# Performance work log

Measured on AMD Instinct MI355X. Metric: run time of the kernel, lower is better.

## Reference

```python
import jax, jax.numpy as jnp
import numpy as np

HIDDEN = 128
HEADS = 8
HEAD_DIM = HIDDEN // HEADS
N = 2048
SCALE = HEAD_DIM ** -0.5


def setup_inputs() -> dict:
    key = jax.random.key(0)
    ks = jax.random.split(key, 12)
    # xavier_uniform bound for square (HIDDEN, HIDDEN) weights
    bound = float(np.sqrt(6.0 / (HIDDEN + HIDDEN)))
    def w(k):
        return jax.random.uniform(k, (HIDDEN, HIDDEN), jnp.float32, -bound, bound)
    return {
        "x": jax.random.normal(ks[0], (N, HIDDEN), jnp.float32),
        "attention_bias": jax.random.normal(ks[1], (N, N, HEADS), jnp.float32),
        "key_padding_mask": jnp.zeros((N,), jnp.bool_),
        "Wq": w(ks[2]), "bq": jnp.zeros((HIDDEN,), jnp.float32),
        "Wk": w(ks[3]), "bk": jnp.zeros((HIDDEN,), jnp.float32),
        "Wv": w(ks[4]), "bv": jnp.zeros((HIDDEN,), jnp.float32),
        "Wo": w(ks[5]), "bo": jnp.zeros((HIDDEN,), jnp.float32),
    }


def reference(x, attention_bias, key_padding_mask, Wq, bq, Wk, bk, Wv, bv, Wo, bo):
    n = x.shape[0]
    # torch Linear: y = x @ W.T + b
    q = (x @ Wq.T + bq).reshape(n, HEADS, HEAD_DIM).transpose(1, 0, 2)  # (H, N, D)
    k = (x @ Wk.T + bk).reshape(n, HEADS, HEAD_DIM).transpose(1, 0, 2)
    v = (x @ Wv.T + bv).reshape(n, HEADS, HEAD_DIM).transpose(1, 0, 2)
    scores = jnp.einsum('hnd,hmd->hnm', q, k) * SCALE        # (H, N, N)
    scores = scores + attention_bias.transpose(2, 0, 1)       # additive graph bias
    mask = key_padding_mask[None, None, :]                    # (1, 1, N) over keys
    scores = jnp.where(mask, -jnp.inf, scores)
    attn = jax.nn.softmax(scores, axis=-1)
    out = jnp.einsum('hnm,hmd->hnd', attn, v)                 # (H, N, D)
    out = out.transpose(1, 0, 2).reshape(n, HIDDEN)
    return out @ Wo.T + bo
```

## Files before the change

### kernel.cpp

```cpp
#include <hip/hip_runtime.h>
#include <hip/hip_bf16.h>

#define NSEQ 2048
#define HID 128
#define HEADS 8
#define HD 16
#define SCALE 0.25f
#define TQ 16
#define SPLIT 16
#define KEYS_PER (NSEQ / SPLIT)
#define KT16 (KEYS_PER / 16)

typedef unsigned short ushort_t;
typedef __attribute__((ext_vector_type(4))) short short4v;
typedef __attribute__((ext_vector_type(4))) float floatx4;

__device__ __forceinline__ unsigned pack_bf16x2(float a, float b) {
    __hip_bfloat16 ba = __float2bfloat16(a);
    __hip_bfloat16 bb = __float2bfloat16(b);
    return (unsigned)*(ushort_t*)&ba | ((unsigned)*(ushort_t*)&bb << 16);
}

__global__ void transpose_kernel(const float* __restrict__ Wq, const float* __restrict__ Wk,
                                 const float* __restrict__ Wv, const float* __restrict__ Wo,
                                 float* __restrict__ wt)
{
    int idx = blockIdx.x * 256 + threadIdx.x;
    int w = idx >> 14, rem = idx & 16383;
    int row = rem >> 7, col = rem & 127;
    const float* W = (w == 0) ? Wq : (w == 1) ? Wk : (w == 2) ? Wv : Wo;
    wt[w * 16384 + col * HID + row] = W[rem];
}

__global__ __launch_bounds__(128) void qkv_kernel(
    const float* __restrict__ x, const float* __restrict__ WqT,
    const float* __restrict__ WkT, const float* __restrict__ WvT,
    const float* __restrict__ bq, const float* __restrict__ bk,
    const float* __restrict__ bv,
    __hip_bfloat16* __restrict__ Qh, __hip_bfloat16* __restrict__ Ql,
    __hip_bfloat16* __restrict__ Kb, __hip_bfloat16* __restrict__ Vt)
{
    __shared__ float xs[8 * HID];
    const int j = threadIdx.x;
    const int mat = blockIdx.x >> 8;
    const int rb = blockIdx.x & 255;
    const int r0 = rb * 8;
    const float* WT = (mat == 0) ? WqT : (mat == 1) ? WkT : WvT;
    const float* bb = (mat == 0) ? bq : (mat == 1) ? bk : bv;
    const float4* xg = (const float4*)(x + (size_t)r0 * HID);
    float4* xl = (float4*)xs;
    for (int i = j; i < 8 * HID / 4; i += 128) xl[i] = xg[i];
    __syncthreads();
    float acc[8];
#pragma unroll
    for (int r = 0; r < 8; ++r) acc[r] = 0.f;
#pragma unroll 4
    for (int i = 0; i < HID; ++i) {
        float w = WT[i * HID + j];
#pragma unroll
        for (int r = 0; r < 8; ++r) acc[r] = fmaf(xs[r * HID + i], w, acc[r]);
    }
    float bv_ = bb[j];
#pragma unroll
    for (int r = 0; r < 8; ++r) acc[r] += bv_;
    if (mat == 0) {
#pragma unroll
        for (int r = 0; r < 8; ++r) {
            float qsv = acc[r] * SCALE;
            __hip_bfloat16 hb = __float2bfloat16(qsv);
            float hf = __bfloat162float(hb);
            __hip_bfloat16 lb = __float2bfloat16(qsv - hf);
            Qh[(size_t)(r0 + r) * HID + j] = hb;
            Ql[(size_t)(r0 + r) * HID + j] = lb;
        }
    } else if (mat == 1) {
#pragma unroll
        for (int r = 0; r < 8; ++r) Kb[(size_t)(r0 + r) * HID + j] = __float2bfloat16(acc[r]);
    } else {
        unsigned u[4];
#pragma unroll
        for (int p = 0; p < 4; ++p) u[p] = pack_bf16x2(acc[2 * p], acc[2 * p + 1]);
        *(uint4*)((ushort_t*)Vt + (size_t)j * NSEQ + r0) = make_uint4(u[0], u[1], u[2], u[3]);
    }
}

__global__ __launch_bounds__(256, 4) void attn_kernel(
    const __hip_bfloat16* __restrict__ Qh, const __hip_bfloat16* __restrict__ Ql,
    const __hip_bfloat16* __restrict__ Kb, const __hip_bfloat16* __restrict__ Vt,
    const float* __restrict__ bias, const unsigned char* __restrict__ mask,
    float* __restrict__ Op, float* __restrict__ Lp)
{
    const int t = threadIdx.x;
    const int lane = t & 63;
    const int wid = t >> 6;
    const int qi = lane & 15;
    const int g = lane >> 4;
    const int qb = blockIdx.x & 127;
    const int sp = blockIdx.x >> 7;
    const int n0 = qb * TQ;
    const int m0 = sp * KEYS_PER;
    const int h0 = wid * 2;

    short4v qhf[2], qlf[2];
#pragma unroll
    for (int hh = 0; hh < 2; ++hh) {
        const size_t qoff = (size_t)(n0 + qi) * HID + (h0 + hh) * HD + 4 * g;
        qhf[hh] = *(const short4v*)((const ushort_t*)Qh + qoff);
        qlf[hh] = *(const short4v*)((const ushort_t*)Ql + qoff);
    }

    floatx4 o[2];
    o[0] = (floatx4){0.f, 0.f, 0.f, 0.f};
    o[1] = (floatx4){0.f, 0.f, 0.f, 0.f};
    float lrun[2] = {0.f, 0.f};

    const float* bias_base = bias + (size_t)(n0 + qi) * NSEQ * HEADS;

#pragma unroll 2
    for (int kt = 0; kt < KT16; ++kt) {
        const int m1 = m0 + kt * 16;
        const uchar4 mk = *(const uchar4*)(mask + m1 + 4 * g);
#pragma unroll
        for (int hh = 0; hh < 2; ++hh) {
            const int h = h0 + hh;
            short4v ka = *(const short4v*)((const ushort_t*)Kb +
                         (size_t)(m1 + qi) * HID + h * HD + 4 * g);
            const float* bp = bias_base + (size_t)(m1 + 4 * g) * HEADS + h;
            floatx4 s;
            s.x = bp[0]; s.y = bp[8]; s.z = bp[16]; s.w = bp[24];
            s = __builtin_amdgcn_mfma_f32_16x16x16bf16_1k(ka, qhf[hh], s, 0, 0, 0);
            s = __builtin_amdgcn_mfma_f32_16x16x16bf16_1k(ka, qlf[hh], s, 0, 0, 0);
            float e0 = mk.x ? 0.f : __expf(s.x);
            float e1 = mk.y ? 0.f : __expf(s.y);
            float e2 = mk.z ? 0.f : __expf(s.z);
            float e3 = mk.w ? 0.f : __expf(s.w);
            lrun[hh] += (e0 + e1) + (e2 + e3);
            __hip_bfloat16 p0 = __float2bfloat16(e0);
            __hip_bfloat16 p1 = __float2bfloat16(e1);
            __hip_bfloat16 p2 = __float2bfloat16(e2);
            __hip_bfloat16 p3 = __float2bfloat16(e3);
            short4v pa = {(short)*(ushort_t*)&p0, (short)*(ushort_t*)&p1,
                          (short)*(ushort_t*)&p2, (short)*(ushort_t*)&p3};
            short4v vb = *(const short4v*)((const ushort_t*)Vt +
                         (size_t)(h * HD + qi) * NSEQ + m1 + 4 * g);
            o[hh] = __builtin_amdgcn_mfma_f32_16x16x16bf16_1k(pa, vb, o[hh], 0, 0, 0);
        }
    }

#pragma unroll
    for (int hh = 0; hh < 2; ++hh) {
        lrun[hh] += __shfl_xor(lrun[hh], 16);
        lrun[hh] += __shfl_xor(lrun[hh], 32);
        const int h = h0 + hh;
#pragma unroll
        for (int r = 0; r < 4; ++r)
            Op[((size_t)sp * NSEQ + n0 + 4 * g + r) * HID + h * HD + qi] = o[hh][r];
        if (g == 0)
            Lp[((size_t)sp * NSEQ + n0 + qi) * HEADS + h] = lrun[hh];
    }
}

__global__ __launch_bounds__(128) void proj_kernel(
    const float* __restrict__ Op, const float* __restrict__ Lp,
    const float* __restrict__ WoT, const float* __restrict__ bo,
    float* __restrict__ out)
{
    __shared__ float xs[4 * HID];
    const int j = threadIdx.x;
    const int r0 = blockIdx.x * 4;
    const int hh = j >> 4;
#pragma unroll
    for (int r = 0; r < 4; ++r) {
        const size_t n = r0 + r;
        float s = 0.f, l = 0.f;
#pragma unroll
        for (int sp = 0; sp < SPLIT; ++sp) {
            s += Op[((size_t)sp * NSEQ + n) * HID + j];
            l += Lp[((size_t)sp * NSEQ + n) * HEADS + hh];
        }
        xs[r * HID + j] = s / l;
    }
    __syncthreads();
    float acc[4];
#pragma unroll
    for (int r = 0; r < 4; ++r) acc[r] = 0.f;
#pragma unroll 4
    for (int i = 0; i < HID; ++i) {
        float w = WoT[i * HID + j];
#pragma unroll
        for (int r = 0; r < 4; ++r) acc[r] = fmaf(xs[r * HID + i], w, acc[r]);
    }
    float b = bo[j];
#pragma unroll
    for (int r = 0; r < 4; ++r)
        out[(size_t)(r0 + r) * HID + j] = acc[r] + b;
}

extern "C" void kernel_launch(void* const* d_in, const int* in_sizes, int n_in,
                              void* d_out, int out_size, void* d_ws, size_t ws_size,
                              hipStream_t stream) {
    const float* x    = (const float*)d_in[0];
    const float* bias = (const float*)d_in[1];
    const unsigned char* mask = (const unsigned char*)d_in[2];
    const float* Wq = (const float*)d_in[3];
    const float* bq = (const float*)d_in[4];
    const float* Wk = (const float*)d_in[5];
    const float* bk = (const float*)d_in[6];
    const float* Wv = (const float*)d_in[7];
    const float* bv = (const float*)d_in[8];
    const float* Wo = (const float*)d_in[9];
    const float* bo = (const float*)d_in[10];
    float* out = (float*)d_out;

    float* w = (float*)d_ws;
    float* WqT = w;
    float* WkT = w + 16384;
    float* WvT = w + 32768;
    float* WoT = w + 49152;
    __hip_bfloat16* Qh = (__hip_bfloat16*)(w + 65536);
    __hip_bfloat16* Ql = (__hip_bfloat16*)(w + 196608);
    __hip_bfloat16* Kb = (__hip_bfloat16*)(w + 327680);
    __hip_bfloat16* Vt = (__hip_bfloat16*)(w + 458752);
    float* Op  = w + 589824;
    float* Lp  = w + 589824 + (size_t)SPLIT * NSEQ * HID;

    transpose_kernel<<<256, 256, 0, stream>>>(Wq, Wk, Wv, Wo, w);
    qkv_kernel<<<768, 128, 0, stream>>>(x, WqT, WkT, WvT, bq, bk, bv, Qh, Ql, Kb, Vt);
    attn_kernel<<<128 * SPLIT, 256, 0, stream>>>(Qh, Ql, Kb, Vt, bias, mask, Op, Lp);
    proj_kernel<<<512, 128, 0, stream>>>(Op, Lp, WoT, bo, out);
}
```

Before: 296.6 us.

## Stage bias via coalesced double-buffered LDS loads, drop weight transpose, halve split

The attention kernel now reads the 128MB bias tensor with coalesced nontemporal float4 loads into a double-buffered shared-memory tile, instead of strided scalar gathers per MFMA fragment. The next tile is prefetched while the current one is consumed. The weight transpose kernel is removed, and the QKV and output projections read untransposed weight rows as float4. SPLIT drops from 16 to 8 and the partial-output layout becomes row-major per query. The changes add a __syncthreads per key tile, raise occupancy hints, and halve the grid size.

```diff
diff --git a/kernel.cpp b/kernel.cpp
--- a/kernel.cpp
+++ b/kernel.cpp
@@ -7,13 +7,15 @@
 #define HD 16
 #define SCALE 0.25f
 #define TQ 16
-#define SPLIT 16
+#define SPLIT 8
 #define KEYS_PER (NSEQ / SPLIT)
 #define KT16 (KEYS_PER / 16)
+#define NS 132
 
 typedef unsigned short ushort_t;
 typedef __attribute__((ext_vector_type(4))) short short4v;
 typedef __attribute__((ext_vector_type(4))) float floatx4;
+typedef __attribute__((ext_vector_type(4))) float f32x4;
 
 __device__ __forceinline__ unsigned pack_bf16x2(float a, float b) {
     __hip_bfloat16 ba = __float2bfloat16(a);
@@ -21,20 +23,9 @@
     return (unsigned)*(ushort_t*)&ba | ((unsigned)*(ushort_t*)&bb << 16);
 }
 
-__global__ void transpose_kernel(const float* __restrict__ Wq, const float* __restrict__ Wk,
-                                 const float* __restrict__ Wv, const float* __restrict__ Wo,
-                                 float* __restrict__ wt)
-{
-    int idx = blockIdx.x * 256 + threadIdx.x;
-    int w = idx >> 14, rem = idx & 16383;
-    int row = rem >> 7, col = rem & 127;
-    const float* W = (w == 0) ? Wq : (w == 1) ? Wk : (w == 2) ? Wv : Wo;
-    wt[w * 16384 + col * HID + row] = W[rem];
-}
-
 __global__ __launch_bounds__(128) void qkv_kernel(
-    const float* __restrict__ x, const float* __restrict__ WqT,
-    const float* __restrict__ WkT, const float* __restrict__ WvT,
+    const float* __restrict__ x, const float* __restrict__ Wq,
+    const float* __restrict__ Wk, const float* __restrict__ Wv,
     const float* __restrict__ bq, const float* __restrict__ bk,
     const float* __restrict__ bv,
     __hip_bfloat16* __restrict__ Qh, __hip_bfloat16* __restrict__ Ql,
@@ -45,7 +36,7 @@
     const int mat = blockIdx.x >> 8;
     const int rb = blockIdx.x & 255;
     const int r0 = rb * 8;
-    const float* WT = (mat == 0) ? WqT : (mat == 1) ? WkT : WvT;
+    const float* W = (mat == 0) ? Wq : (mat == 1) ? Wk : Wv;
     const float* bb = (mat == 0) ? bq : (mat == 1) ? bk : bv;
     const float4* xg = (const float4*)(x + (size_t)r0 * HID);
     float4* xl = (float4*)xs;
@@ -54,11 +45,18 @@
     float acc[8];
 #pragma unroll
     for (int r = 0; r < 8; ++r) acc[r] = 0.f;
+    const float4* Wrow = (const float4*)(W + (size_t)j * HID);
 #pragma unroll 4
-    for (int i = 0; i < HID; ++i) {
-        float w = WT[i * HID + j];
-#pragma unroll
-        for (int r = 0; r < 8; ++r) acc[r] = fmaf(xs[r * HID + i], w, acc[r]);
+    for (int i4 = 0; i4 < HID / 4; ++i4) {
+        float4 wv = Wrow[i4];
+#pragma unroll
+        for (int r = 0; r < 8; ++r) {
+            float4 xv = *(const float4*)&xs[r * HID + i4 * 4];
+            acc[r] = fmaf(xv.x, wv.x, acc[r]);
+            acc[r] = fmaf(xv.y, wv.y, acc[r]);
+            acc[r] = fmaf(xv.z, wv.z, acc[r]);
+            acc[r] = fmaf(xv.w, wv.w, acc[r]);
+        }
     }
     float bv_ = bb[j];
 #pragma unroll
@@ -84,12 +82,14 @@
     }
 }
 
-__global__ __launch_bounds__(256, 4) void attn_kernel(
+__global__ __launch_bounds__(256, 6) void attn_kernel(
     const __hip_bfloat16* __restrict__ Qh, const __hip_bfloat16* __restrict__ Ql,
     const __hip_bfloat16* __restrict__ Kb, const __hip_bfloat16* __restrict__ Vt,
     const float* __restrict__ bias, const unsigned char* __restrict__ mask,
     float* __restrict__ Op, float* __restrict__ Lp)
 {
+    __shared__ float bs[2][16 * NS];
+
     const int t = threadIdx.x;
     const int lane = t & 63;
     const int wid = t >> 6;
@@ -101,6 +101,11 @@
     const int m0 = sp * KEYS_PER;
     const int h0 = wid * 2;
 
+    const int sn = t >> 4;
+    const int sc = t & 15;
+    const float* brow = bias + (size_t)(n0 + sn) * (NSEQ * HEADS) + (size_t)(m0 + sc) * HEADS;
+    const int wbase = sn * NS + sc;
+
     short4v qhf[2], qlf[2];
 #pragma unroll
     for (int hh = 0; hh < 2; ++hh) {
@@ -114,10 +119,22 @@
     o[1] = (floatx4){0.f, 0.f, 0.f, 0.f};
     float lrun[2] = {0.f, 0.f};
 
-    const float* bias_base = bias + (size_t)(n0 + qi) * NSEQ * HEADS;
+    f32x4 st0 = __builtin_nontemporal_load((const f32x4*)brow);
+    f32x4 st1 = __builtin_nontemporal_load((const f32x4*)(brow + 4));
 
 #pragma unroll 2
     for (int kt = 0; kt < KT16; ++kt) {
+        float* B = &bs[kt & 1][0];
+        B[wbase]       = st0.x; B[wbase + 16]  = st0.y;
+        B[wbase + 32]  = st0.z; B[wbase + 48]  = st0.w;
+        B[wbase + 64]  = st1.x; B[wbase + 80]  = st1.y;
+        B[wbase + 96]  = st1.z; B[wbase + 112] = st1.w;
+        __syncthreads();
+        if (kt + 1 < KT16) {
+            const float* bnext = brow + (size_t)(kt + 1) * 16 * HEADS;
+            st0 = __builtin_nontemporal_load((const f32x4*)bnext);
+            st1 = __builtin_nontemporal_load((const f32x4*)(bnext + 4));
+        }
         const int m1 = m0 + kt * 16;
         const uchar4 mk = *(const uchar4*)(mask + m1 + 4 * g);
 #pragma unroll
@@ -125,9 +142,7 @@
             const int h = h0 + hh;
             short4v ka = *(const short4v*)((const ushort_t*)Kb +
                          (size_t)(m1 + qi) * HID + h * HD + 4 * g);
-            const float* bp = bias_base + (size_t)(m1 + 4 * g) * HEADS + h;
-            floatx4 s;
-            s.x = bp[0]; s.y = bp[8]; s.z = bp[16]; s.w = bp[24];
+            floatx4 s = *(const f32x4*)&B[qi * NS + h * 16 + 4 * g];
             s = __builtin_amdgcn_mfma_f32_16x16x16bf16_1k(ka, qhf[hh], s, 0, 0, 0);
             s = __builtin_amdgcn_mfma_f32_16x16x16bf16_1k(ka, qlf[hh], s, 0, 0, 0);
             float e0 = mk.x ? 0.f : __expf(s.x);
@@ -154,15 +169,15 @@
         const int h = h0 + hh;
 #pragma unroll
         for (int r = 0; r < 4; ++r)
-            Op[((size_t)sp * NSEQ + n0 + 4 * g + r) * HID + h * HD + qi] = o[hh][r];
+            Op[((size_t)(n0 + 4 * g + r) * SPLIT + sp) * HID + h * HD + qi] = o[hh][r];
         if (g == 0)
-            Lp[((size_t)sp * NSEQ + n0 + qi) * HEADS + h] = lrun[hh];
+            Lp[((size_t)(n0 + qi) * SPLIT + sp) * HEADS + h] = lrun[hh];
     }
 }
 
 __global__ __launch_bounds__(128) void proj_kernel(
     const float* __restrict__ Op, const float* __restrict__ Lp,
-    const float* __restrict__ WoT, const float* __restrict__ bo,
+    const float* __restrict__ Wo, const float* __restrict__ bo,
     float* __restrict__ out)
 {
     __shared__ float xs[4 * HID];
@@ -175,8 +190,8 @@
         float s = 0.f, l = 0.f;
 #pragma unroll
         for (int sp = 0; sp < SPLIT; ++sp) {
-            s += Op[((size_t)sp * NSEQ + n) * HID + j];
-            l += Lp[((size_t)sp * NSEQ + n) * HEADS + hh];
+            s += Op[(n * SPLIT + sp) * HID + j];
+            l += Lp[(n * SPLIT + sp) * HEADS + hh];
         }
         xs[r * HID + j] = s / l;
     }
@@ -184,11 +199,18 @@
     float acc[4];
 #pragma unroll
     for (int r = 0; r < 4; ++r) acc[r] = 0.f;
+    const float4* Wrow = (const float4*)(Wo + (size_t)j * HID);
 #pragma unroll 4
-    for (int i = 0; i < HID; ++i) {
-        float w = WoT[i * HID + j];
-#pragma unroll
-        for (int r = 0; r < 4; ++r) acc[r] = fmaf(xs[r * HID + i], w, acc[r]);
+    for (int i4 = 0; i4 < HID / 4; ++i4) {
+        float4 wv = Wrow[i4];
+#pragma unroll
+        for (int r = 0; r < 4; ++r) {
+            float4 xv = *(const float4*)&xs[r * HID + i4 * 4];
+            acc[r] = fmaf(xv.x, wv.x, acc[r]);
+            acc[r] = fmaf(xv.y, wv.y, acc[r]);
+            acc[r] = fmaf(xv.z, wv.z, acc[r]);
+            acc[r] = fmaf(xv.w, wv.w, acc[r]);
+        }
     }
     float b = bo[j];
 #pragma unroll
@@ -213,19 +235,14 @@
     float* out = (float*)d_out;
 
     float* w = (float*)d_ws;
-    float* WqT = w;
-    float* WkT = w + 16384;
-    float* WvT = w + 32768;
-    float* WoT = w + 49152;
-    __hip_bfloat16* Qh = (__hip_bfloat16*)(w + 65536);
-    __hip_bfloat16* Ql = (__hip_bfloat16*)(w + 196608);
-    __hip_bfloat16* Kb = (__hip_bfloat16*)(w + 327680);
-    __hip_bfloat16* Vt = (__hip_bfloat16*)(w + 458752);
-    float* Op  = w + 589824;
-    float* Lp  = w + 589824 + (size_t)SPLIT * NSEQ * HID;
-
-    transpose_kernel<<<256, 256, 0, stream>>>(Wq, Wk, Wv, Wo, w);
-    qkv_kernel<<<768, 128, 0, stream>>>(x, WqT, WkT, WvT, bq, bk, bv, Qh, Ql, Kb, Vt);
+    __hip_bfloat16* Qh = (__hip_bfloat16*)(w);
+    __hip_bfloat16* Ql = (__hip_bfloat16*)(w + 131072);
+    __hip_bfloat16* Kb = (__hip_bfloat16*)(w + 262144);
+    __hip_bfloat16* Vt = (__hip_bfloat16*)(w + 393216);
+    float* Op  = w + 524288;
+    float* Lp  = w + 524288 + (size_t)NSEQ * SPLIT * HID;
+
+    qkv_kernel<<<768, 128, 0, stream>>>(x, Wq, Wk, Wv, bq, bk, bv, Qh, Ql, Kb, Vt);
     attn_kernel<<<128 * SPLIT, 256, 0, stream>>>(Qh, Ql, Kb, Vt, bias, mask, Op, Lp);
-    proj_kernel<<<512, 128, 0, stream>>>(Op, Lp, WoT, bo, out);
-}
+    proj_kernel<<<512, 128, 0, stream>>>(Op, Lp, Wo, bo, out);
+}
```

Result: faster. 255.7 us (-13.8%).
